# Optimization experiments

Hardware: AMD Instinct MI355X
Metric: run time of the kernel (lower is better)

Reference implementation:

```python
import jax, jax.numpy as jnp
import numpy as np

V, D, NH, T_MAX, L, MLP = 50257, 1024, 16, 1024, 12, 4
HD = D // NH
F = D * MLP
B, T = 2, 1024


def setup_inputs() -> dict:
    key = jax.random.key(0)
    ks = jax.random.split(key, 16)
    s = 0.02
    inp = {
        'tokens': jax.random.randint(ks[0], (B, T), 0, V, dtype=jnp.int32),
        'wte': jax.random.normal(ks[1], (V, D), jnp.float32) * s,
        'wpe': jax.random.normal(ks[2], (T_MAX, D), jnp.float32) * s,
        'ln1_w': jnp.ones((L, D)), 'ln1_b': jnp.zeros((L, D)),
        'attn_w': jax.random.normal(ks[3], (L, D, 3 * D), jnp.float32) * s,
        'attn_b': jnp.zeros((L, 3 * D)),
        'aproj_w': jax.random.normal(ks[4], (L, D, D), jnp.float32) * s,
        'aproj_b': jnp.zeros((L, D)),
        'ln2_w': jnp.ones((L, D)), 'ln2_b': jnp.zeros((L, D)),
        'fc_w': jax.random.normal(ks[5], (L, D, F), jnp.float32) * s,
        'fc_b': jnp.zeros((L, F)),
        'proj_w': jax.random.normal(ks[6], (L, F, D), jnp.float32) * s,
        'proj_b': jnp.zeros((L, D)),
        'lnf_w': jnp.ones((D,)), 'lnf_b': jnp.zeros((D,)),
    }
    return inp


def _ln(x, w, b, eps=1e-5):
    m = jnp.mean(x, -1, keepdims=True)
    v = jnp.var(x, -1, keepdims=True)
    return (x - m) * jax.lax.rsqrt(v + eps) * w + b


def _forward(tokens, wte, wpe, ln1_w, ln1_b, attn_w, attn_b, aproj_w, aproj_b,
             ln2_w, ln2_b, fc_w, fc_b, proj_w, proj_b, lnf_w, lnf_b):
    b, t = tokens.shape
    x = wte[tokens] + wpe[:t]  # [B,T,D]
    scale = HD ** -0.5
    causal = jnp.tril(jnp.ones((t, t), bool))  # [T,T]

    def block(x, p):
        l1w, l1b, aw, ab, apw, apb, l2w, l2b, fw, fb, pw, pb = p
        h = _ln(x, l1w, l1b)
        qkv = h @ aw + ab  # [B,T,3D]
        q, k, v = jnp.split(qkv, 3, axis=-1)
        # rearrange 'b t (h n) -> b n t h' with n=NH: last dim is (head_size, n_heads)
        def split_heads(u):
            return u.reshape(b, t, HD, NH).transpose(0, 3, 1, 2)  # [B,NH,T,HD]
        q, k, v = split_heads(q), split_heads(k), split_heads(v)
        scores = jnp.einsum('bnth,bnsh->bnts', q, k) * scale
        scores = jnp.where(causal, scores, -jnp.inf)
        w = jax.nn.softmax(scores, axis=-1)
        att = jnp.einsum('bnts,bnsh->bnth', w, v)
        # rearrange 'b n t h -> b t (n h)'
        att = att.transpose(0, 2, 1, 3).reshape(b, t, D)
        x = x + (att @ apw + apb)
        h2 = _ln(x, l2w, l2b)
        x = x + (jax.nn.gelu(h2 @ fw + fb, approximate=False) @ pw + pb)
        return x, None

    params = (ln1_w, ln1_b, attn_w, attn_b, aproj_w, aproj_b,
              ln2_w, ln2_b, fc_w, fc_b, proj_w, proj_b)
    x, _ = jax.lax.scan(block, x, params)
    x = _ln(x, lnf_w, lnf_b)[:, -1:, :]  # [B,1,D]
    return x @ wte.T  # tied lm_head -> [B,1,V]


def reference(tokens, wte, wpe, ln1_w, ln1_b, attn_w, attn_b, aproj_w, aproj_b,
              ln2_w, ln2_b, fc_w, fc_b, proj_w, proj_b, lnf_w, lnf_b):
    return _forward(tokens, wte, wpe, ln1_w, ln1_b, attn_w, attn_b, aproj_w,
                    aproj_b, ln2_w, ln2_b, fc_w, fc_b, proj_w, proj_b, lnf_w, lnf_b)
```

## Files before the change

### kernel.cpp

```cpp
#include <hip/hip_runtime.h>
#include <cstdint>
#include <math.h>


using u16 = unsigned short;
using bf16x8 = __attribute__((ext_vector_type(8))) short;
using f32x4 = __attribute__((ext_vector_type(4))) float;

#define GLDS16(g, l)                                                        \
  __builtin_amdgcn_global_load_lds(                                         \
      (const __attribute__((address_space(1))) void*)(g),                   \
      (__attribute__((address_space(3))) void*)(l), 16, 0, 0)

__device__ __forceinline__ u16 f2bf(float f) {
  union { float f; unsigned u; } t; t.f = f;
  unsigned r = t.u + 0x7fffu + ((t.u >> 16) & 1u);
  return (u16)(r >> 16);
}
__device__ __forceinline__ float bf2f(u16 v) {
  union { unsigned u; float f; } t; t.u = ((unsigned)v) << 16;
  return t.f;
}

__device__ __forceinline__ float fast_erf(float x) {
  float ax = fabsf(x);
  float t = 1.f / (1.f + 0.3275911f * ax);
  float y = t * (0.254829592f +
            t * (-0.284496736f +
            t * (1.421413741f +
            t * (-1.453152027f +
            t * 1.061405429f))));
  float r = 1.f - y * __expf(-ax * ax);
  return copysignf(r, x);
}

#define DD 1024
#define TTT 1024
#define MR 2048
#define FFF 4096
#define VVV 50257

__global__ __launch_bounds__(256) void k_embed(const int* __restrict__ tokens,
                                               const float* __restrict__ wte,
                                               const float* __restrict__ wpe,
                                               float* __restrict__ x) {
  int m = blockIdx.x, d = threadIdx.x * 4;
  int t = m & (TTT - 1);
  int tok = tokens[m];
  const float4 a = *(const float4*)(wte + (size_t)tok * DD + d);
  const float4 p = *(const float4*)(wpe + (size_t)t * DD + d);
  float4 o; o.x = a.x + p.x; o.y = a.y + p.y; o.z = a.z + p.z; o.w = a.w + p.w;
  *(float4*)(x + (size_t)m * DD + d) = o;
}

__device__ __forceinline__ void addln_body(float* __restrict__ x,
                                           const u16* __restrict__ pp, int npart,
                                           const float* __restrict__ w,
                                           const float* __restrict__ b,
                                           u16* __restrict__ out, int blk) {
  const int wid = threadIdx.x >> 6, lane = threadIdx.x & 63;
  const int m = blk * 4 + wid;
  float* row = x + (size_t)m * DD;
  float4 v[4];
  float s = 0.f, q = 0.f;
#pragma unroll
  for (int j = 0; j < 4; ++j) {
    v[j] = *(const float4*)(row + j * 256 + lane * 4);
#pragma unroll 4
    for (int p = 0; p < npart; ++p) {
      uint64_t pv = *(const uint64_t*)(pp + (size_t)p * MR * DD + (size_t)m * DD + j * 256 + lane * 4);
      v[j].x += bf2f((u16)(pv));
      v[j].y += bf2f((u16)(pv >> 16));
      v[j].z += bf2f((u16)(pv >> 32));
      v[j].w += bf2f((u16)(pv >> 48));
    }
    if (npart) *(float4*)(row + j * 256 + lane * 4) = v[j];
    s += v[j].x + v[j].y + v[j].z + v[j].w;
    q += v[j].x * v[j].x + v[j].y * v[j].y + v[j].z * v[j].z + v[j].w * v[j].w;
  }
#pragma unroll
  for (int off = 1; off < 64; off <<= 1) { s += __shfl_xor(s, off); q += __shfl_xor(q, off); }
  float mean = s * (1.f / DD);
  float var = q * (1.f / DD) - mean * mean;
  float rs = rsqrtf(var + 1e-5f);
#pragma unroll
  for (int j = 0; j < 4; ++j) {
    const float4 wv = *(const float4*)(w + j * 256 + lane * 4);
    const float4 bv = *(const float4*)(b + j * 256 + lane * 4);
    u16 o[4];
    o[0] = f2bf((v[j].x - mean) * rs * wv.x + bv.x);
    o[1] = f2bf((v[j].y - mean) * rs * wv.y + bv.y);
    o[2] = f2bf((v[j].z - mean) * rs * wv.z + bv.z);
    o[3] = f2bf((v[j].w - mean) * rs * wv.w + bv.w);
    *(uint64_t*)(out + (size_t)m * DD + j * 256 + lane * 4) = *(uint64_t*)o;
  }
}

__global__ __launch_bounds__(256) void k_addln(float* __restrict__ x,
                                               const u16* __restrict__ pp, int npart,
                                               const float* __restrict__ w,
                                               const float* __restrict__ b,
                                               u16* __restrict__ out) {
  addln_body(x, pp, npart, w, b, out, blockIdx.x);
}

__device__ __forceinline__ void wtrans_body(const float* __restrict__ atw,
                                            const float* __restrict__ apw,
                                            const float* __restrict__ fcw,
                                            const float* __restrict__ pjw,
                                            u16* __restrict__ wt, int id) {
  __shared__ u16 tb[64][72];
  const float* W; u16* Wt; int K, N, local, kts; bool perm = false;
  if (id < 768)       { W = atw; Wt = wt;           K = 1024; N = 3072; local = id;        kts = 4; perm = true; }
  else if (id < 1024) { W = apw; Wt = wt + 3145728; K = 1024; N = 1024; local = id - 768;  kts = 4; }
  else if (id < 2048) { W = fcw; Wt = wt + 4194304; K = 1024; N = 4096; local = id - 1024; kts = 4; }
  else                { W = pjw; Wt = wt + 8388608; K = 4096; N = 1024; local = id - 2048; kts = 6; }
  const int k0 = (local & ((1 << kts) - 1)) * 64, n0 = (local >> kts) * 64;
  const int tid = threadIdx.x;
  const int rr = tid >> 4, c4 = (tid & 15) * 4;
#pragma unroll
  for (int i = 0; i < 4; ++i) {
    const int r = rr + i * 16;
    const float4 v = *(const float4*)(W + (size_t)(k0 + r) * N + n0 + c4);
    tb[c4 + 0][r] = f2bf(v.x);
    tb[c4 + 1][r] = f2bf(v.y);
    tb[c4 + 2][r] = f2bf(v.z);
    tb[c4 + 3][r] = f2bf(v.w);
  }
  __syncthreads();
  const int n = tid >> 3, k8 = (tid & 7) * 8;
#pragma unroll
  for (int s = 0; s < 2; ++s) {
    u16 o[8];
#pragma unroll
    for (int j = 0; j < 8; ++j) o[j] = tb[n + s * 32][k8 + j];
    int orow = n0 + n + s * 32;
    if (perm) {
      int part = orow >> 10, w = orow & 1023;
      orow = part * 1024 + (w & 15) * 64 + (w >> 4);
    }
    *(bf16x8*)(Wt + (size_t)orow * K + k0 + k8) = *(bf16x8*)o;
  }
}

__global__ __launch_bounds__(256) void k_prep(float* __restrict__ x,
                                              const u16* __restrict__ pp, int npart,
                                              const float* __restrict__ w,
                                              const float* __restrict__ b,
                                              u16* __restrict__ out,
                                              const float* __restrict__ atw,
                                              const float* __restrict__ apw,
                                              const float* __restrict__ fcw,
                                              const float* __restrict__ pjw,
                                              u16* __restrict__ wt,
                                              const float* __restrict__ ab,
                                              float* __restrict__ pbias) {
  if (blockIdx.x < 512) {
    addln_body(x, pp, npart, w, b, out, blockIdx.x);
  } else if (blockIdx.x == 3584) {
    for (int c = threadIdx.x; c < 3072; c += 256) {
      int part = c >> 10, ww = c & 1023;
      pbias[c] = ab[part * 1024 + (ww & 63) * 16 + (ww >> 6)];
    }
  } else {
    wtrans_body(atw, apw, fcw, pjw, wt, blockIdx.x - 512);
  }
}

template <int EPI>
__global__ __launch_bounds__(256) void k_gemm(const u16* __restrict__ A,
                                              const u16* __restrict__ Bt,
                                              const float* __restrict__ bias,
                                              u16* __restrict__ outb,
                                              u16* __restrict__ pp,
                                              int M, int N, int K, int KC) {
  __shared__ u16 smem[4][128 * 64];
  const int nbx = gridDim.x, nby = gridDim.y;
  const int nwg = nbx * nby * gridDim.z;
  const int orig = blockIdx.x + nbx * (blockIdx.y + nby * blockIdx.z);
  const int qq = nwg >> 3, rr = nwg & 7;
  const int xcd = orig & 7, pos = orig >> 3;
  const int wg = (xcd < rr ? xcd * (qq + 1) : rr * (qq + 1) + (xcd - rr) * qq) + pos;
  const int bx = wg % nbx;
  const int tmpw = wg / nbx;
  const int by = tmpw % nby, bz = tmpw / nby;

  const int tid = threadIdx.x;
  const int lane = tid & 63, wid = tid >> 6;
  const int wr = wid >> 1, wc = wid & 1;
  const int l15 = lane & 15, l4 = lane >> 4;
  const int sx = l15 & 7;
  const int m0 = bx * 128, n0 = by * 128;
  f32x4 acc[4][4] = {};

  const int srow = tid >> 3;
  const int scol = (((tid & 7) ^ (srow & 7)) * 8);
  const int k0beg = bz * KC;
  const int nt = KC >> 6;

  const u16* Ap = A + (size_t)(m0 + srow) * K + scol;
  const u16* Bp = Bt + (size_t)(n0 + srow) * K + scol;

#define STAGE(buf, k0)                                                      \
  {                                                                         \
    _Pragma("unroll")                                                       \
    for (int it = 0; it < 4; ++it) {                                        \
      GLDS16(Ap + (size_t)it * 32 * K + (k0), (char*)smem[buf] + it * 4096 + tid * 16); \
      GLDS16(Bp + (size_t)it * 32 * K + (k0), (char*)smem[2 + (buf)] + it * 4096 + tid * 16); \
    }                                                                       \
  }

  STAGE(0, k0beg);
  for (int t = 0; t < nt; ++t) {
    if (t + 1 < nt) {
      STAGE((t + 1) & 1, k0beg + (t + 1) * 64);
      asm volatile("s_waitcnt vmcnt(8)" ::: "memory");
    } else {
      asm volatile("s_waitcnt vmcnt(0)" ::: "memory");
    }
    __builtin_amdgcn_sched_barrier(0);
    __builtin_amdgcn_s_barrier();
    __builtin_amdgcn_sched_barrier(0);
    const u16* Ab = smem[t & 1];
    const u16* Bb = smem[2 + (t & 1)];
#pragma unroll
    for (int ks = 0; ks < 2; ++ks) {
      const int ch = ((ks * 4 + l4) ^ sx) * 8;
      bf16x8 af[4], bfr[4];
#pragma unroll
      for (int i = 0; i < 4; ++i)
        af[i] = *(const bf16x8*)(Ab + (wr * 64 + i * 16 + l15) * 64 + ch);
#pragma unroll
      for (int j = 0; j < 4; ++j)
        bfr[j] = *(const bf16x8*)(Bb + (wc * 64 + j * 16 + l15) * 64 + ch);
      __builtin_amdgcn_s_setprio(1);
#pragma unroll
      for (int i = 0; i < 4; ++i)
#pragma unroll
        for (int j = 0; j < 4; ++j)
          acc[i][j] = __builtin_amdgcn_mfma_f32_16x16x32_bf16(af[i], bfr[j], acc[i][j], 0, 0, 0);
      __builtin_amdgcn_s_setprio(0);
    }
    __builtin_amdgcn_sched_barrier(0);
    __builtin_amdgcn_s_barrier();
    __builtin_amdgcn_sched_barrier(0);
  }
#undef STAGE
  u16* eb = (u16*)smem;
#pragma unroll
  for (int j = 0; j < 4; ++j) {
    const int col = wc * 64 + j * 16 + l15;
    const float bs = (EPI == 4 && bz != 0) ? 0.f : bias[n0 + col];
#pragma unroll
    for (int i = 0; i < 4; ++i) {
#pragma unroll
      for (int r = 0; r < 4; ++r) {
        const int row = wr * 64 + i * 16 + l4 * 4 + r;
        float v = acc[i][j][r] + bs;
        if (EPI == 2) v = 0.5f * v * (1.f + fast_erf(v * 0.70710678118f));
        eb[row * 132 + col] = f2bf(v);
      }
    }
  }
  __syncthreads();
  const int erow = tid >> 1;
  const int ecol0 = (tid & 1) * 64;
  u16* gout = (EPI == 4) ? (pp + (size_t)bz * M * N) : outb;
  u16* gdst = gout + (size_t)(m0 + erow) * N + n0 + ecol0;
  const u16* esrc = eb + erow * 132 + ecol0;
#pragma unroll
  for (int c = 0; c < 8; ++c)
    *(bf16x8*)(gdst + c * 8) = *(const bf16x8*)(esrc + c * 8);
}

__global__ __launch_bounds__(256) void k_repack(const u16* __restrict__ qkv,
                                                u16* __restrict__ Vt) {
  __shared__ u16 tile[16][1032];
  const int tid = threadIdx.x;
  const int m0 = blockIdx.x * 16;
  const int b = m0 >> 10;
  const int tg0 = m0 & (TTT - 1);
#pragma unroll
  for (int p = 0; p < 8; ++p) {
    int row = p * 2 + (tid >> 7);
    int col8 = (tid & 127) * 8;
    bf16x8 v = *(const bf16x8*)(qkv + (size_t)(m0 + row) * 3072 + 2048 + col8);
    *(bf16x8*)(&tile[row][col8]) = v;
  }
  __syncthreads();
  const int lane = tid & 63, wid = tid >> 6;
  for (int p = wid; p < 32; p += 4) {
    int n = p >> 1, tc = p & 1;
    u16 o[8];
#pragma unroll
    for (int k = 0; k < 8; ++k) o[k] = tile[tc * 8 + k][n * 64 + lane];
    *(bf16x8*)(Vt + (((size_t)(b * 16 + n)) * 64 + lane) * TTT + tg0 + tc * 8) =
        *(bf16x8*)o;
  }
}

__global__ __launch_bounds__(256) void k_attn(const u16* __restrict__ qkv,
                                              const u16* __restrict__ Vt,
                                              u16* __restrict__ attout) {
  __shared__ u16 Ks[128 * 64];
  __shared__ u16 Vs[64 * 128];
  __shared__ u16 Ps[4][16 * 136];

  const int tid = threadIdx.x;
  const int lane = tid & 63, wid = tid >> 6;
  const int l15 = lane & 15, l4 = lane >> 4;
  const int bn = blockIdx.x;
  const int b = bn >> 4, nh = bn & 15;
  const char* Kg0 = (const char*)(qkv + (size_t)b * TTT * 3072 + 1024 + nh * 64);
  const char* Vg0 = (const char*)(Vt + (size_t)bn * 64 * TTT);

#pragma unroll
  for (int pass = 0; pass < 2; ++pass) {
    const int qtr = pass == 0 ? 15 - (int)blockIdx.y : (int)blockIdx.y;
    const int q0 = qtr * 64;

    const int qrow = q0 + wid * 16 + l15;
    const u16* qsrc = qkv + (size_t)(b * TTT + qrow) * 3072 + nh * 64;
    bf16x8 aq[2];
#pragma unroll
    for (int ks = 0; ks < 2; ++ks)
      aq[ks] = *(const bf16x8*)(qsrc + ks * 32 + l4 * 8);

    float m_run[4], l_part[4];
    f32x4 o[4] = {};
#pragma unroll
    for (int r = 0; r < 4; ++r) { m_run[r] = -1e30f; l_part[r] = 0.f; }

    const int ntk = (qtr >> 1) + 1;
    for (int kt = 0; kt < ntk; ++kt) {
#pragma unroll
      for (int it = 0; it < 4; ++it) {
        int L = it * 4096 + tid * 16;
        int Ls = L ^ (((L >> 7) & 7) << 4);
        int krow = Ls >> 7, cb = Ls & 127;
        GLDS16(Kg0 + (size_t)(kt * 128 + krow) * 6144 + cb, (char*)Ks + L);
      }
#pragma unroll
      for (int it = 0; it < 4; ++it) {
        int L = it * 4096 + tid * 16;
        int Ls = L ^ (((L >> 8) & 7) << 4);
        int hrow = Ls >> 8, cb = Ls & 255;
        GLDS16(Vg0 + (size_t)hrow * 2048 + kt * 256 + cb, (char*)Vs + L);
      }
      __syncthreads();

      f32x4 sf[8];
#pragma unroll
      for (int cf = 0; cf < 8; ++cf) {
        f32x4 z = {};
#pragma unroll
        for (int ks = 0; ks < 2; ++ks) {
          int P = (cf * 16 + l15) * 128 + (ks * 32 + l4 * 8) * 2;
          bf16x8 kb = *(const bf16x8*)((const char*)Ks + (P ^ (((P >> 7) & 7) << 4)));
          z = __builtin_amdgcn_mfma_f32_16x16x32_bf16(aq[ks], kb, z, 0, 0, 0);
        }
        sf[cf] = z;
      }
      const bool lastkt = (kt == ntk - 1);
#pragma unroll
      for (int cf = 0; cf < 8; ++cf)
#pragma unroll
        for (int r = 0; r < 4; ++r) {
          float s = sf[cf][r] * 0.125f;
          if (lastkt) {
            int kg = kt * 128 + cf * 16 + l15;
            int qg = q0 + wid * 16 + l4 * 4 + r;
            if (kg > qg) s = -1e30f;
          }
          sf[cf][r] = s;
        }
      float fac[4];
#pragma unroll
      for (int r = 0; r < 4; ++r) {
        float tm = sf[0][r];
#pragma unroll
        for (int cf = 1; cf < 8; ++cf) tm = fmaxf(tm, sf[cf][r]);
#pragma unroll
        for (int off = 1; off < 16; off <<= 1) tm = fmaxf(tm, __shfl_xor(tm, off));
        float mnew = fmaxf(m_run[r], tm);
        fac[r] = __expf(m_run[r] - mnew);
        m_run[r] = mnew;
        float ps = 0.f;
#pragma unroll
        for (int cf = 0; cf < 8; ++cf) {
          float p = __expf(sf[cf][r] - mnew);
          sf[cf][r] = p;
          ps += p;
        }
        l_part[r] = l_part[r] * fac[r] + ps;
      }
#pragma unroll
      for (int cf = 0; cf < 8; ++cf)
#pragma unroll
        for (int r = 0; r < 4; ++r)
          Ps[wid][(l4 * 4 + r) * 136 + cf * 16 + l15] = f2bf(sf[cf][r]);
#pragma unroll
      for (int hf = 0; hf < 4; ++hf)
#pragma unroll
        for (int r = 0; r < 4; ++r) o[hf][r] *= fac[r];
      bf16x8 pa[4];
#pragma unroll
      for (int ks = 0; ks < 4; ++ks)
        pa[ks] = *(const bf16x8*)&Ps[wid][l15 * 136 + ks * 32 + l4 * 8];
#pragma unroll
      for (int hf = 0; hf < 4; ++hf) {
#pragma unroll
        for (int ks = 0; ks < 4; ++ks) {
          int P = (hf * 16 + l15) * 256 + (ks * 32 + l4 * 8) * 2;
          bf16x8 vb = *(const bf16x8*)((const char*)Vs + (P ^ (((P >> 8) & 7) << 4)));
          o[hf] = __builtin_amdgcn_mfma_f32_16x16x32_bf16(pa[ks], vb, o[hf], 0, 0, 0);
        }
      }
      __syncthreads();
    }
    float lsum[4];
#pragma unroll
    for (int r = 0; r < 4; ++r) {
      float s = l_part[r];
#pragma unroll
      for (int off = 1; off < 16; off <<= 1) s += __shfl_xor(s, off);
      lsum[r] = s;
    }
#pragma unroll
    for (int hf = 0; hf < 4; ++hf)
#pragma unroll
      for (int r = 0; r < 4; ++r) {
        float val = o[hf][r] / lsum[r];
        size_t row = (size_t)b * TTT + q0 + wid * 16 + l4 * 4 + r;
        attout[row * DD + nh * 64 + hf * 16 + l15] = f2bf(val);
      }
  }
}

__global__ __launch_bounds__(256) void k_head(const float* __restrict__ x,
                                              const u16* __restrict__ pp, int npart,
                                              const float* __restrict__ lnf_w,
                                              const float* __restrict__ lnf_b,
                                              const float* __restrict__ wte,
                                              float* __restrict__ out) {
  __shared__ float xs[2 * DD];
  __shared__ float sm[8];
  int tid = threadIdx.x;
  int wid = tid >> 6, lane = tid & 63;
#pragma unroll
  for (int bb = 0; bb < 2; ++bb) {
    int m = bb * TTT + (TTT - 1);
    float4 v = *(const float4*)(x + (size_t)m * DD + tid * 4);
#pragma unroll 4
    for (int p = 0; p < npart; ++p) {
      uint64_t pv = *(const uint64_t*)(pp + (size_t)p * MR * DD + (size_t)m * DD + tid * 4);
      v.x += bf2f((u16)(pv));
      v.y += bf2f((u16)(pv >> 16));
      v.z += bf2f((u16)(pv >> 32));
      v.w += bf2f((u16)(pv >> 48));
    }
    float s = v.x + v.y + v.z + v.w;
    float q = v.x * v.x + v.y * v.y + v.z * v.z + v.w * v.w;
#pragma unroll
    for (int off = 1; off < 64; off <<= 1) { s += __shfl_xor(s, off); q += __shfl_xor(q, off); }
    if ((tid & 63) == 0) { sm[wid] = s; sm[4 + wid] = q; }
    __syncthreads();
    s = sm[0] + sm[1] + sm[2] + sm[3];
    q = sm[4] + sm[5] + sm[6] + sm[7];
    float mean = s * (1.f / DD);
    float var = q * (1.f / DD) - mean * mean;
    float rs = rsqrtf(var + 1e-5f);
    const float4 wv = *(const float4*)(lnf_w + tid * 4);
    const float4 bv = *(const float4*)(lnf_b + tid * 4);
    float4 o;
    o.x = (v.x - mean) * rs * wv.x + bv.x;
    o.y = (v.y - mean) * rs * wv.y + bv.y;
    o.z = (v.z - mean) * rs * wv.z + bv.z;
    o.w = (v.w - mean) * rs * wv.w + bv.w;
    *(float4*)(xs + bb * DD + tid * 4) = o;
    __syncthreads();
  }
  for (int v = blockIdx.x * 4 + wid; v < VVV; v += gridDim.x * 4) {
    const float* wr = wte + (size_t)v * DD;
    float a0 = 0.f, a1 = 0.f;
#pragma unroll
    for (int j = 0; j < 4; ++j) {
      const float4 wv = *(const float4*)(wr + lane * 16 + j * 4);
      const float4 x0 = *(const float4*)(xs + lane * 16 + j * 4);
      const float4 x1 = *(const float4*)(xs + DD + lane * 16 + j * 4);
      a0 += wv.x * x0.x + wv.y * x0.y + wv.z * x0.z + wv.w * x0.w;
      a1 += wv.x * x1.x + wv.y * x1.y + wv.z * x1.z + wv.w * x1.w;
    }
#pragma unroll
    for (int off = 1; off < 64; off <<= 1) { a0 += __shfl_xor(a0, off); a1 += __shfl_xor(a1, off); }
    if (lane == 0) { out[v] = a0; out[VVV + v] = a1; }
  }
}

extern "C" void kernel_launch(void* const* d_in, const int* in_sizes, int n_in,
                              void* d_out, int out_size, void* d_ws, size_t ws_size,
                              hipStream_t stream) {
  const int* tokens    = (const int*)d_in[0];
  const float* wte     = (const float*)d_in[1];
  const float* wpe     = (const float*)d_in[2];
  const float* ln1_w   = (const float*)d_in[3];
  const float* ln1_b   = (const float*)d_in[4];
  const float* attn_w  = (const float*)d_in[5];
  const float* attn_b  = (const float*)d_in[6];
  const float* aproj_w = (const float*)d_in[7];
  const float* aproj_b = (const float*)d_in[8];
  const float* ln2_w   = (const float*)d_in[9];
  const float* ln2_b   = (const float*)d_in[10];
  const float* fc_w    = (const float*)d_in[11];
  const float* fc_b    = (const float*)d_in[12];
  const float* proj_w  = (const float*)d_in[13];
  const float* proj_b  = (const float*)d_in[14];
  const float* lnf_w   = (const float*)d_in[15];
  const float* lnf_b   = (const float*)d_in[16];

  char* ws = (char*)d_ws;
  float* x    = (float*)(ws);
  u16* h      = (u16*)(ws + (8u << 20));
  u16* wt     = (u16*)(ws + (12u << 20));
  u16* qkv    = (u16*)(ws + (36u << 20));
  u16* Vt     = (u16*)(ws + (52u << 20));
  u16* attb   = (u16*)(ws + (56u << 20));
  u16* mlph   = (u16*)(ws + (36u << 20));
  u16* pp     = (u16*)(ws + (60u << 20));
  float* pbias = (float*)(ws + (92u << 20));
  float* out  = (float*)d_out;

  u16* atw = wt;
  u16* apw = wt + 3145728;
  u16* fcw = wt + 4194304;
  u16* pjw = wt + 8388608;

  k_embed<<<MR, 256, 0, stream>>>(tokens, wte, wpe, x);

  for (int l = 0; l < 12; ++l) {
    k_prep<<<3585, 256, 0, stream>>>(x, pp, l == 0 ? 0 : 4,
                                     ln1_w + l * DD, ln1_b + l * DD, h,
                                     attn_w + (size_t)l * DD * 3 * DD,
                                     aproj_w + (size_t)l * DD * DD,
                                     fc_w + (size_t)l * DD * FFF,
                                     proj_w + (size_t)l * FFF * DD, wt,
                                     attn_b + (size_t)l * 3 * DD, pbias);
    k_gemm<0><<<dim3(16, 24, 1), 256, 0, stream>>>(h, atw, pbias, qkv, nullptr, MR, 3072, 1024, 1024);
    k_repack<<<128, 256, 0, stream>>>(qkv, Vt);
    k_attn<<<dim3(32, 8), 256, 0, stream>>>(qkv, Vt, attb);
    k_gemm<4><<<dim3(16, 8, 4), 256, 0, stream>>>(attb, apw, aproj_b + (size_t)l * DD, nullptr, pp, MR, 1024, 1024, 256);
    k_addln<<<512, 256, 0, stream>>>(x, pp, 4, ln2_w + l * DD, ln2_b + l * DD, h);
    k_gemm<2><<<dim3(16, 32, 1), 256, 0, stream>>>(h, fcw, fc_b + (size_t)l * FFF, mlph, nullptr, MR, 4096, 1024, 1024);
    k_gemm<4><<<dim3(16, 8, 4), 256, 0, stream>>>(mlph, pjw, proj_b + (size_t)l * DD, nullptr, pp, MR, 1024, 4096, 1024);
  }
  k_head<<<512, 256, 0, stream>>>(x, pp, 4, lnf_w, lnf_b, wte, out);
}
```

Measured before the change: 1.837 ms.

## Fuse V transpose into QKV GEMM epilogue and simplify attention softmax

The QKV GEMM epilogue now writes the V columns directly in transposed per-head layout, which removes the separate repack kernel launch and its extra read and write of V. The attention kernel drops the two-pass paired query tiles and instead launches one block per query tile, doubling the grid, so causal load balancing now relies on the scheduler. The softmax switches to exp2 with a folded scale and only rescales the running max when it grows by a threshold, which skips rescale work. The deferred rescale lets exponentials grow up to a bounded factor, which carries some risk to precision.

```diff
diff --git a/kernel.cpp b/kernel.cpp
--- a/kernel.cpp
+++ b/kernel.cpp
@@ -173,6 +173,7 @@
                                               const float* __restrict__ bias,
                                               u16* __restrict__ outb,
                                               u16* __restrict__ pp,
+                                              u16* __restrict__ vt,
                                               int M, int N, int K, int KC) {
   __shared__ u16 smem[4][128 * 64];
   const int nbx = gridDim.x, nby = gridDim.y;
@@ -263,39 +264,30 @@
     }
   }
   __syncthreads();
-  const int erow = tid >> 1;
-  const int ecol0 = (tid & 1) * 64;
-  u16* gout = (EPI == 4) ? (pp + (size_t)bz * M * N) : outb;
-  u16* gdst = gout + (size_t)(m0 + erow) * N + n0 + ecol0;
-  const u16* esrc = eb + erow * 132 + ecol0;
-#pragma unroll
-  for (int c = 0; c < 8; ++c)
-    *(bf16x8*)(gdst + c * 8) = *(const bf16x8*)(esrc + c * 8);
-}
-
-__global__ __launch_bounds__(256) void k_repack(const u16* __restrict__ qkv,
-                                                u16* __restrict__ Vt) {
-  __shared__ u16 tile[16][1032];
-  const int tid = threadIdx.x;
-  const int m0 = blockIdx.x * 16;
-  const int b = m0 >> 10;
-  const int tg0 = m0 & (TTT - 1);
-#pragma unroll
-  for (int p = 0; p < 8; ++p) {
-    int row = p * 2 + (tid >> 7);
-    int col8 = (tid & 127) * 8;
-    bf16x8 v = *(const bf16x8*)(qkv + (size_t)(m0 + row) * 3072 + 2048 + col8);
-    *(bf16x8*)(&tile[row][col8]) = v;
-  }
-  __syncthreads();
-  const int lane = tid & 63, wid = tid >> 6;
-  for (int p = wid; p < 32; p += 4) {
-    int n = p >> 1, tc = p & 1;
-    u16 o[8];
-#pragma unroll
-    for (int k = 0; k < 8; ++k) o[k] = tile[tc * 8 + k][n * 64 + lane];
-    *(bf16x8*)(Vt + (((size_t)(b * 16 + n)) * 64 + lane) * TTT + tg0 + tc * 8) =
-        *(bf16x8*)o;
+  if (EPI == 0 && by >= 16) {
+    const int b = m0 >> 10, t0 = m0 & 1023;
+    const int col = tid >> 1;
+    const int tseg = tid & 1;
+    const int gc = n0 + col - 2048;
+    const int n = gc >> 6, hh = gc & 63;
+    u16* vdst = vt + (((size_t)(b * 16 + n)) * 64 + hh) * TTT + t0 + tseg * 64;
+    const u16* es = eb + (tseg * 64) * 132 + col;
+#pragma unroll
+    for (int s = 0; s < 8; ++s) {
+      u16 o[8];
+#pragma unroll
+      for (int k = 0; k < 8; ++k) o[k] = es[(s * 8 + k) * 132];
+      *(bf16x8*)(vdst + s * 8) = *(bf16x8*)o;
+    }
+  } else {
+    const int erow = tid >> 1;
+    const int ecol0 = (tid & 1) * 64;
+    u16* gout = (EPI == 4) ? (pp + (size_t)bz * M * N) : outb;
+    u16* gdst = gout + (size_t)(m0 + erow) * N + n0 + ecol0;
+    const u16* esrc = eb + erow * 132 + ecol0;
+#pragma unroll
+    for (int c = 0; c < 8; ++c)
+      *(bf16x8*)(gdst + c * 8) = *(const bf16x8*)(esrc + c * 8);
   }
 }
 
@@ -310,131 +302,127 @@
   const int lane = tid & 63, wid = tid >> 6;
   const int l15 = lane & 15, l4 = lane >> 4;
   const int bn = blockIdx.x;
+  const int qtr = 15 - (int)blockIdx.y;
+  const int q0 = qtr * 64;
   const int b = bn >> 4, nh = bn & 15;
   const char* Kg0 = (const char*)(qkv + (size_t)b * TTT * 3072 + 1024 + nh * 64);
   const char* Vg0 = (const char*)(Vt + (size_t)bn * 64 * TTT);
-
-#pragma unroll
-  for (int pass = 0; pass < 2; ++pass) {
-    const int qtr = pass == 0 ? 15 - (int)blockIdx.y : (int)blockIdx.y;
-    const int q0 = qtr * 64;
-
-    const int qrow = q0 + wid * 16 + l15;
-    const u16* qsrc = qkv + (size_t)(b * TTT + qrow) * 3072 + nh * 64;
-    bf16x8 aq[2];
-#pragma unroll
-    for (int ks = 0; ks < 2; ++ks)
-      aq[ks] = *(const bf16x8*)(qsrc + ks * 32 + l4 * 8);
-
-    float m_run[4], l_part[4];
-    f32x4 o[4] = {};
-#pragma unroll
-    for (int r = 0; r < 4; ++r) { m_run[r] = -1e30f; l_part[r] = 0.f; }
-
-    const int ntk = (qtr >> 1) + 1;
-    for (int kt = 0; kt < ntk; ++kt) {
-#pragma unroll
-      for (int it = 0; it < 4; ++it) {
-        int L = it * 4096 + tid * 16;
-        int Ls = L ^ (((L >> 7) & 7) << 4);
-        int krow = Ls >> 7, cb = Ls & 127;
-        GLDS16(Kg0 + (size_t)(kt * 128 + krow) * 6144 + cb, (char*)Ks + L);
+  const float CEXP = 0.125f * 1.44269504f;
+
+  const int qrow = q0 + wid * 16 + l15;
+  const u16* qsrc = qkv + (size_t)(b * TTT + qrow) * 3072 + nh * 64;
+  bf16x8 aq[2];
+#pragma unroll
+  for (int ks = 0; ks < 2; ++ks)
+    aq[ks] = *(const bf16x8*)(qsrc + ks * 32 + l4 * 8);
+
+  float m_run[4], l_part[4];
+  f32x4 o[4] = {};
+#pragma unroll
+  for (int r = 0; r < 4; ++r) { m_run[r] = -1e30f; l_part[r] = 0.f; }
+
+  const int ntk = (qtr >> 1) + 1;
+  for (int kt = 0; kt < ntk; ++kt) {
+#pragma unroll
+    for (int it = 0; it < 4; ++it) {
+      int L = it * 4096 + tid * 16;
+      int Ls = L ^ (((L >> 7) & 7) << 4);
+      int krow = Ls >> 7, cb = Ls & 127;
+      GLDS16(Kg0 + (size_t)(kt * 128 + krow) * 6144 + cb, (char*)Ks + L);
+    }
+#pragma unroll
+    for (int it = 0; it < 4; ++it) {
+      int L = it * 4096 + tid * 16;
+      int Ls = L ^ (((L >> 8) & 7) << 4);
+      int hrow = Ls >> 8, cb = Ls & 255;
+      GLDS16(Vg0 + (size_t)hrow * 2048 + kt * 256 + cb, (char*)Vs + L);
+    }
+    __syncthreads();
+
+    f32x4 sf[8];
+#pragma unroll
+    for (int cf = 0; cf < 8; ++cf) {
+      f32x4 z = {};
+#pragma unroll
+      for (int ks = 0; ks < 2; ++ks) {
+        int P = (cf * 16 + l15) * 128 + (ks * 32 + l4 * 8) * 2;
+        bf16x8 kb = *(const bf16x8*)((const char*)Ks + (P ^ (((P >> 7) & 7) << 4)));
+        z = __builtin_amdgcn_mfma_f32_16x16x32_bf16(aq[ks], kb, z, 0, 0, 0);
       }
-#pragma unroll
-      for (int it = 0; it < 4; ++it) {
-        int L = it * 4096 + tid * 16;
-        int Ls = L ^ (((L >> 8) & 7) << 4);
-        int hrow = Ls >> 8, cb = Ls & 255;
-        GLDS16(Vg0 + (size_t)hrow * 2048 + kt * 256 + cb, (char*)Vs + L);
+      sf[cf] = z;
+    }
+    if (kt == ntk - 1) {
+#pragma unroll
+      for (int cf = 0; cf < 8; ++cf)
+#pragma unroll
+        for (int r = 0; r < 4; ++r) {
+          int kg = kt * 128 + cf * 16 + l15;
+          int qg = q0 + wid * 16 + l4 * 4 + r;
+          if (kg > qg) sf[cf][r] = -1e30f;
+        }
+    }
+    float fac[4];
+#pragma unroll
+    for (int r = 0; r < 4; ++r) {
+      float tm = fmaxf(fmaxf(fmaxf(sf[0][r], sf[1][r]), fmaxf(sf[2][r], sf[3][r])),
+                       fmaxf(fmaxf(sf[4][r], sf[5][r]), fmaxf(sf[6][r], sf[7][r])));
+#pragma unroll
+      for (int off = 1; off < 16; off <<= 1) tm = fmaxf(tm, __shfl_xor(tm, off));
+      if (tm > m_run[r] + 64.f) {
+        fac[r] = exp2f((m_run[r] - tm) * CEXP);
+        m_run[r] = tm;
+      } else {
+        fac[r] = 1.f;
       }
-      __syncthreads();
-
-      f32x4 sf[8];
+      float ps = 0.f;
 #pragma unroll
       for (int cf = 0; cf < 8; ++cf) {
-        f32x4 z = {};
-#pragma unroll
-        for (int ks = 0; ks < 2; ++ks) {
-          int P = (cf * 16 + l15) * 128 + (ks * 32 + l4 * 8) * 2;
-          bf16x8 kb = *(const bf16x8*)((const char*)Ks + (P ^ (((P >> 7) & 7) << 4)));
-          z = __builtin_amdgcn_mfma_f32_16x16x32_bf16(aq[ks], kb, z, 0, 0, 0);
-        }
-        sf[cf] = z;
+        float p = exp2f((sf[cf][r] - m_run[r]) * CEXP);
+        sf[cf][r] = p;
+        ps += p;
       }
-      const bool lastkt = (kt == ntk - 1);
-#pragma unroll
-      for (int cf = 0; cf < 8; ++cf)
-#pragma unroll
-        for (int r = 0; r < 4; ++r) {
-          float s = sf[cf][r] * 0.125f;
-          if (lastkt) {
-            int kg = kt * 128 + cf * 16 + l15;
-            int qg = q0 + wid * 16 + l4 * 4 + r;
-            if (kg > qg) s = -1e30f;
-          }
-          sf[cf][r] = s;
-        }
-      float fac[4];
-#pragma unroll
-      for (int r = 0; r < 4; ++r) {
-        float tm = sf[0][r];
-#pragma unroll
-        for (int cf = 1; cf < 8; ++cf) tm = fmaxf(tm, sf[cf][r]);
-#pragma unroll
-        for (int off = 1; off < 16; off <<= 1) tm = fmaxf(tm, __shfl_xor(tm, off));
-        float mnew = fmaxf(m_run[r], tm);
-        fac[r] = __expf(m_run[r] - mnew);
-        m_run[r] = mnew;
-        float ps = 0.f;
-#pragma unroll
-        for (int cf = 0; cf < 8; ++cf) {
-          float p = __expf(sf[cf][r] - mnew);
-          sf[cf][r] = p;
-          ps += p;
-        }
-        l_part[r] = l_part[r] * fac[r] + ps;
+      l_part[r] = l_part[r] * fac[r] + ps;
+    }
+#pragma unroll
+    for (int cf = 0; cf < 8; ++cf)
+#pragma unroll
+      for (int r = 0; r < 4; ++r)
+        Ps[wid][(l4 * 4 + r) * 136 + cf * 16 + l15] = f2bf(sf[cf][r]);
+#pragma unroll
+    for (int hf = 0; hf < 4; ++hf)
+#pragma unroll
+      for (int r = 0; r < 4; ++r) o[hf][r] *= fac[r];
+    bf16x8 pa[4];
+#pragma unroll
+    for (int ks = 0; ks < 4; ++ks)
+      pa[ks] = *(const bf16x8*)&Ps[wid][l15 * 136 + ks * 32 + l4 * 8];
+#pragma unroll
+    for (int hf = 0; hf < 4; ++hf) {
+#pragma unroll
+      for (int ks = 0; ks < 4; ++ks) {
+        int P = (hf * 16 + l15) * 256 + (ks * 32 + l4 * 8) * 2;
+        bf16x8 vb = *(const bf16x8*)((const char*)Vs + (P ^ (((P >> 8) & 7) << 4)));
+        o[hf] = __builtin_amdgcn_mfma_f32_16x16x32_bf16(pa[ks], vb, o[hf], 0, 0, 0);
       }
-#pragma unroll
-      for (int cf = 0; cf < 8; ++cf)
-#pragma unroll
-        for (int r = 0; r < 4; ++r)
-          Ps[wid][(l4 * 4 + r) * 136 + cf * 16 + l15] = f2bf(sf[cf][r]);
-#pragma unroll
-      for (int hf = 0; hf < 4; ++hf)
-#pragma unroll
-        for (int r = 0; r < 4; ++r) o[hf][r] *= fac[r];
-      bf16x8 pa[4];
-#pragma unroll
-      for (int ks = 0; ks < 4; ++ks)
-        pa[ks] = *(const bf16x8*)&Ps[wid][l15 * 136 + ks * 32 + l4 * 8];
-#pragma unroll
-      for (int hf = 0; hf < 4; ++hf) {
-#pragma unroll
-        for (int ks = 0; ks < 4; ++ks) {
-          int P = (hf * 16 + l15) * 256 + (ks * 32 + l4 * 8) * 2;
-          bf16x8 vb = *(const bf16x8*)((const char*)Vs + (P ^ (((P >> 8) & 7) << 4)));
-          o[hf] = __builtin_amdgcn_mfma_f32_16x16x32_bf16(pa[ks], vb, o[hf], 0, 0, 0);
-        }
-      }
-      __syncthreads();
-    }
-    float lsum[4];
+    }
+    __syncthreads();
+  }
+  float lsum[4];
+#pragma unroll
+  for (int r = 0; r < 4; ++r) {
+    float s = l_part[r];
+#pragma unroll
+    for (int off = 1; off < 16; off <<= 1) s += __shfl_xor(s, off);
+    lsum[r] = s;
+  }
+#pragma unroll
+  for (int hf = 0; hf < 4; ++hf)
 #pragma unroll
     for (int r = 0; r < 4; ++r) {
-      float s = l_part[r];
-#pragma unroll
-      for (int off = 1; off < 16; off <<= 1) s += __shfl_xor(s, off);
-      lsum[r] = s;
-    }
-#pragma unroll
-    for (int hf = 0; hf < 4; ++hf)
-#pragma unroll
-      for (int r = 0; r < 4; ++r) {
-        float val = o[hf][r] / lsum[r];
-        size_t row = (size_t)b * TTT + q0 + wid * 16 + l4 * 4 + r;
-        attout[row * DD + nh * 64 + hf * 16 + l15] = f2bf(val);
-      }
-  }
+      float val = o[hf][r] / lsum[r];
+      size_t row = (size_t)b * TTT + q0 + wid * 16 + l4 * 4 + r;
+      attout[row * DD + nh * 64 + hf * 16 + l15] = f2bf(val);
+    }
 }
 
 __global__ __launch_bounds__(256) void k_head(const float* __restrict__ x,
@@ -545,13 +533,12 @@
                                      fc_w + (size_t)l * DD * FFF,
                                      proj_w + (size_t)l * FFF * DD, wt,
                                      attn_b + (size_t)l * 3 * DD, pbias);
-    k_gemm<0><<<dim3(16, 24, 1), 256, 0, stream>>>(h, atw, pbias, qkv, nullptr, MR, 3072, 1024, 1024);
-    k_repack<<<128, 256, 0, stream>>>(qkv, Vt);
-    k_attn<<<dim3(32, 8), 256, 0, stream>>>(qkv, Vt, attb);
-    k_gemm<4><<<dim3(16, 8, 4), 256, 0, stream>>>(attb, apw, aproj_b + (size_t)l * DD, nullptr, pp, MR, 1024, 1024, 256);
+    k_gemm<0><<<dim3(16, 24, 1), 256, 0, stream>>>(h, atw, pbias, qkv, nullptr, Vt, MR, 3072, 1024, 1024);
+    k_attn<<<dim3(32, 16), 256, 0, stream>>>(qkv, Vt, attb);
+    k_gemm<4><<<dim3(16, 8, 4), 256, 0, stream>>>(attb, apw, aproj_b + (size_t)l * DD, nullptr, pp, nullptr, MR, 1024, 1024, 256);
     k_addln<<<512, 256, 0, stream>>>(x, pp, 4, ln2_w + l * DD, ln2_b + l * DD, h);
-    k_gemm<2><<<dim3(16, 32, 1), 256, 0, stream>>>(h, fcw, fc_b + (size_t)l * FFF, mlph, nullptr, MR, 4096, 1024, 1024);
-    k_gemm<4><<<dim3(16, 8, 4), 256, 0, stream>>>(mlph, pjw, proj_b + (size_t)l * DD, nullptr, pp, MR, 1024, 4096, 1024);
+    k_gemm<2><<<dim3(16, 32, 1), 256, 0, stream>>>(h, fcw, fc_b + (size_t)l * FFF, mlph, nullptr, nullptr, MR, 4096, 1024, 1024);
+    k_gemm<4><<<dim3(16, 8, 4), 256, 0, stream>>>(mlph, pjw, proj_b + (size_t)l * DD, nullptr, pp, nullptr, MR, 1024, 4096, 1024);
   }
   k_head<<<512, 256, 0, stream>>>(x, pp, 4, lnf_w, lnf_b, wte, out);
 }
```

Result: faster. 1.765 ms (-4.0%).
